# Kernel tuning notes

Hardware: AMD Instinct MI355X
Metric: run time of the kernel (lower is better)

## Reference

```python
import jax, jax.numpy as jnp
import numpy as np

B, S, D, H, AD, E = 4, 2048, 1024, 2048, 128, 8

def _ln(x, g, b, eps=1e-5):
    m = jnp.mean(x, axis=-1, keepdims=True)
    v = jnp.var(x, axis=-1, keepdims=True)
    return (x - m) * jax.lax.rsqrt(v + eps) * g + b

def setup_inputs() -> dict:
    key = jax.random.key(0)
    ks = jax.random.split(key, 12)
    scale = 1.0 / D ** 0.5
    ascale = scale * 0.01
    ead = 0.01 / AD ** 0.5
    return {
        'x': jax.random.normal(ks[0], (B, S, D), jnp.float32),
        'expert_weights': jax.random.uniform(ks[1], (B, S, E), jnp.float32),
        'Wu': jax.random.normal(ks[2], (H, D), jnp.float32) * scale,
        'bu': jnp.zeros((H,), jnp.float32),
        'Wg': jax.random.normal(ks[3], (H, D), jnp.float32) * scale,
        'bg': jnp.zeros((H,), jnp.float32),
        'Wd': jax.random.normal(ks[4], (D, H), jnp.float32) * scale,
        'bd': jnp.zeros((D,), jnp.float32),
        'Wpre': jax.random.normal(ks[5], (AD, D), jnp.float32) * ascale,
        'bpre': jnp.zeros((AD,), jnp.float32),
        'Wpost': jax.random.normal(ks[6], (AD, H), jnp.float32) * ascale,
        'bpost': jnp.zeros((AD,), jnp.float32),
        'ln_g': jnp.ones((AD,), jnp.float32),
        'ln_b': jnp.zeros((AD,), jnp.float32),
        'Wap': jax.random.normal(ks[7], (H, AD), jnp.float32) * ascale,
        'A': jax.random.normal(ks[8], (E, AD, AD), jnp.float32) * ead,
        'eg': jnp.ones((E, AD), jnp.float32),
        'eb': jnp.zeros((E, AD), jnp.float32),
        'Wp': jax.random.normal(ks[9], (H, AD), jnp.float32) * ead,
        'Wo': jax.random.normal(ks[10], (D, H), jnp.float32) * ead,
    }

def reference(x, expert_weights, Wu, bu, Wg, bg, Wd, bd, Wpre, bpre, Wpost, bpost, ln_g, ln_b, Wap, A, eg, eb, Wp, Wo):
    # ---- SharedExpertMLP ----
    up = x @ Wu.T + bu                      # [B,S,H]
    gate = x @ Wg.T + bg
    hidden = jax.nn.silu(gate) * up
    adapt_in = _ln(x @ Wpre.T + bpre, ln_g, ln_b)        # [B,S,AD]
    adapt_out = _ln(hidden @ Wpost.T + bpost, ln_g, ln_b)
    aw = jnp.einsum('bsa,bta->bst', adapt_in, adapt_out)  # [B,S,S]
    aw = jax.nn.silu(jnp.clip(aw, -5.0, 5.0))
    adapt = jnp.einsum('bst,bta->bsa', aw, adapt_in)
    hidden = hidden + 0.1 * (adapt @ Wap.T)
    shared = hidden @ Wd.T + bd                           # [B,S,D]
    # ---- expert branch (vectorized over experts) ----
    pre = x @ Wpre.T + bpre                               # [B,S,AD] (no adapt_norm here, as in torch)
    h = jnp.einsum('bsa,eca->ebsc', pre, A)               # per-expert adapter linear
    h = _ln(h, eg[:, None, None, :], eb[:, None, None, :])
    wmask = jnp.where(expert_weights > 0, expert_weights, 0.0)  # [B,S,E]
    hw = jnp.einsum('ebsa,bse->bsa', h, wmask)            # weighted combine before shared projections
    Wc = Wo @ Wp                                          # [D,AD]: output_proj(expert_proj(.))
    contrib = hw @ Wc.T                                   # [B,S,D]
    # sum_i w_i * (shared + 0.1*mask_i*expert_i) = shared*sum(w) + 0.1*sum(w_i*expert_i)
    return shared * jnp.sum(expert_weights, axis=-1, keepdims=True) + 0.1 * contrib
```

## Files before the change

kernel.cpp:

```cpp
#include <hip/hip_runtime.h>
#include <math.h>

#define BB 4
#define SS 2048
#define DD 1024
#define HH 2048
#define AD 128
#define EE 8
#define MM (BB*SS)
#define PS 136

typedef unsigned short u16;
typedef short bf16x8 __attribute__((ext_vector_type(8)));
typedef float f32x4 __attribute__((ext_vector_type(4)));
typedef float f32x16 __attribute__((ext_vector_type(16)));

__device__ __forceinline__ float silu_f(float x){ return x / (1.f + __expf(-x)); }

__device__ __forceinline__ u16 f2bf(float f){
    union { float f; unsigned u; } c; c.f = f;
    unsigned r = (c.u + 0x7FFFu + ((c.u >> 16) & 1u)) >> 16;
    return (u16)r;
}

__device__ __forceinline__ void gld16(const u16* g, u16* l){
    __builtin_amdgcn_global_load_lds((const __attribute__((address_space(1))) void*)g,
                                     (__attribute__((address_space(3))) void*)l, 16, 0, 0);
}

__global__ __launch_bounds__(256,2) void mfma_sk(
    const u16* __restrict__ A, const u16* __restrict__ B, float* __restrict__ P,
    int M, int K, int S, long sA, long sB, long sC, long sSplit)
{
    __shared__ __align__(16) u16 As[128*32];
    __shared__ __align__(16) u16 Bs[128*32];
    const int t = threadIdx.x;
    const int lane = t & 63;
    const int wv = t >> 6;
    const int s = blockIdx.x;
    const int m0 = blockIdx.y * 128;
    const u16* Ab = A + (long)blockIdx.z * sA;
    const u16* Bb = B + (long)blockIdx.z * sB;
    const int srow = t >> 2, scol = (t & 3) * 8;
    const int Ks = K / S, kBeg = s * Ks;
    const u16* ga0 = Ab + (long)(m0 + srow) * K + scol + kBeg;
    const u16* ga1 = ga0 + 64L * K;
    const u16* gb0 = Bb + (long)srow * K + scol + kBeg;
    const u16* gb1 = gb0 + 64L * K;
    u16* la0 = As + t * 8;  u16* la1 = As + 2048 + t * 8;
    u16* lb0 = Bs + t * 8;  u16* lb1 = Bs + 2048 + t * 8;
    const int fr = lane & 15, q = lane >> 4;
    const int wm = (wv & 1) * 64, wn = (wv >> 1) * 64;

    f32x4 acc[4][4] = {};
    for (int k0 = 0; k0 < Ks; k0 += 32) {
        gld16(ga0 + k0, la0);
        gld16(ga1 + k0, la1);
        gld16(gb0 + k0, lb0);
        gld16(gb1 + k0, lb1);
        __syncthreads();
        bf16x8 af[4], bfr[4];
        #pragma unroll
        for (int i = 0; i < 4; ++i) af[i]  = *(const bf16x8*)&As[(wm + i*16 + fr)*32 + q*8];
        #pragma unroll
        for (int i = 0; i < 4; ++i) bfr[i] = *(const bf16x8*)&Bs[(wn + i*16 + fr)*32 + q*8];
        #pragma unroll
        for (int mi = 0; mi < 4; ++mi)
            #pragma unroll
            for (int ni = 0; ni < 4; ++ni)
                acc[mi][ni] = __builtin_amdgcn_mfma_f32_16x16x32_bf16(af[mi], bfr[ni], acc[mi][ni], 0, 0, 0);
        __syncthreads();
    }

    float* Pf = P + (long)s * sSplit + (long)blockIdx.z * sC;
    #pragma unroll
    for (int mi = 0; mi < 4; ++mi)
        #pragma unroll
        for (int ni = 0; ni < 4; ++ni) {
            const int col = wn + ni*16 + fr;
            #pragma unroll
            for (int r = 0; r < 4; ++r) {
                const int row = m0 + wm + mi*16 + q*4 + r;
                Pf[(long)row * 128 + col] = acc[mi][ni][r];
            }
        }
}

__global__ __launch_bounds__(256,2) void mfma_upgate(
    const u16* __restrict__ X, const u16* __restrict__ Wu_, const u16* __restrict__ Wg_,
    const float* __restrict__ bu, const float* __restrict__ bg, u16* __restrict__ H)
{
    __shared__ __align__(16) u16 Xs[128*32];
    __shared__ __align__(16) u16 Us[128*32];
    __shared__ __align__(16) u16 Gs[128*32];
    const int t = threadIdx.x, lane = t & 63, wv = t >> 6;
    const int m0 = blockIdx.y * 128, n0 = blockIdx.x * 128;
    const int srow = t >> 2, scol = (t & 3) * 8;
    const u16* gx0 = X   + (long)(m0 + srow) * DD + scol;
    const u16* gx1 = gx0 + 64L * DD;
    const u16* gu0 = Wu_ + (long)(n0 + srow) * DD + scol;
    const u16* gu1 = gu0 + 64L * DD;
    const u16* gg0 = Wg_ + (long)(n0 + srow) * DD + scol;
    const u16* gg1 = gg0 + 64L * DD;
    const int l31 = lane & 31, kh = lane >> 5;
    const int wm = (wv & 1) * 64, wn = (wv >> 1) * 64;

    f32x16 accu[2][2] = {};
    f32x16 accg[2][2] = {};
    for (int k0 = 0; k0 < DD; k0 += 32) {
        gld16(gx0 + k0, Xs + t*8);
        gld16(gx1 + k0, Xs + 2048 + t*8);
        gld16(gu0 + k0, Us + t*8);
        gld16(gu1 + k0, Us + 2048 + t*8);
        gld16(gg0 + k0, Gs + t*8);
        gld16(gg1 + k0, Gs + 2048 + t*8);
        __syncthreads();
        bf16x8 xf[2][2], uf[2][2], gf[2][2];
        #pragma unroll
        for (int mt = 0; mt < 2; ++mt)
            #pragma unroll
            for (int ks = 0; ks < 2; ++ks) {
                xf[mt][ks] = *(const bf16x8*)&Xs[(wm + mt*32 + l31)*32 + ks*16 + kh*8];
                uf[mt][ks] = *(const bf16x8*)&Us[(wn + mt*32 + l31)*32 + ks*16 + kh*8];
                gf[mt][ks] = *(const bf16x8*)&Gs[(wn + mt*32 + l31)*32 + ks*16 + kh*8];
            }
        #pragma unroll
        for (int mt = 0; mt < 2; ++mt)
            #pragma unroll
            for (int nt = 0; nt < 2; ++nt)
                #pragma unroll
                for (int ks = 0; ks < 2; ++ks) {
                    accu[mt][nt] = __builtin_amdgcn_mfma_f32_32x32x16_bf16(xf[mt][ks], uf[nt][ks], accu[mt][nt], 0, 0, 0);
                    accg[mt][nt] = __builtin_amdgcn_mfma_f32_32x32x16_bf16(xf[mt][ks], gf[nt][ks], accg[mt][nt], 0, 0, 0);
                }
        __syncthreads();
    }
    #pragma unroll
    for (int mt = 0; mt < 2; ++mt)
        #pragma unroll
        for (int nt = 0; nt < 2; ++nt) {
            const int col = n0 + wn + nt*32 + l31;
            #pragma unroll
            for (int r = 0; r < 16; ++r) {
                const int row = m0 + wm + mt*32 + (r & 3) + 8*(r >> 2) + 4*kh;
                const float u = accu[mt][nt][r] + bu[col];
                const float g = accg[mt][nt][r] + bg[col];
                H[(long)row * HH + col] = f2bf(silu_f(g) * u);
            }
        }
}

__global__ __launch_bounds__(256,2) void mfma_final(
    const u16* __restrict__ Hh, const u16* __restrict__ Wd_,
    const u16* __restrict__ Ac, const u16* __restrict__ Wcat,
    const float* __restrict__ bd, const float* __restrict__ sumw,
    float* __restrict__ out)
{
    __shared__ __align__(16) u16 As[128*32];
    __shared__ __align__(16) u16 Bs[128*32];
    const int t = threadIdx.x, lane = t & 63, wv = t >> 6;
    const int m0 = blockIdx.y * 128, n0 = blockIdx.x * 128;
    const int srow = t >> 2, scol = (t & 3) * 8;
    const int l31 = lane & 31, kh = lane >> 5;
    const int wm = (wv & 1) * 64, wn = (wv >> 1) * 64;
    u16* la0 = As + t * 8;  u16* la1 = As + 2048 + t * 8;
    u16* lb0 = Bs + t * 8;  u16* lb1 = Bs + 2048 + t * 8;

    f32x16 acc[2][2] = {};
    {
        const u16* ga0 = Hh  + (long)(m0 + srow) * HH + scol;
        const u16* ga1 = ga0 + 64L * HH;
        const u16* gb0 = Wd_ + (long)(n0 + srow) * HH + scol;
        const u16* gb1 = gb0 + 64L * HH;
        for (int k0 = 0; k0 < HH; k0 += 32) {
            gld16(ga0 + k0, la0);
            gld16(ga1 + k0, la1);
            gld16(gb0 + k0, lb0);
            gld16(gb1 + k0, lb1);
            __syncthreads();
            bf16x8 af[2][2], bf[2][2];
            #pragma unroll
            for (int mt = 0; mt < 2; ++mt)
                #pragma unroll
                for (int ks = 0; ks < 2; ++ks) {
                    af[mt][ks] = *(const bf16x8*)&As[(wm + mt*32 + l31)*32 + ks*16 + kh*8];
                    bf[mt][ks] = *(const bf16x8*)&Bs[(wn + mt*32 + l31)*32 + ks*16 + kh*8];
                }
            #pragma unroll
            for (int mt = 0; mt < 2; ++mt)
                #pragma unroll
                for (int nt = 0; nt < 2; ++nt)
                    #pragma unroll
                    for (int ks = 0; ks < 2; ++ks)
                        acc[mt][nt] = __builtin_amdgcn_mfma_f32_32x32x16_bf16(af[mt][ks], bf[nt][ks], acc[mt][nt], 0, 0, 0);
            __syncthreads();
        }
    }
    f32x16 acc2[2][2] = {};
    {
        const u16* ga0 = Ac   + (long)(m0 + srow) * 256 + scol;
        const u16* ga1 = ga0 + 64L * 256;
        const u16* gb0 = Wcat + (long)(n0 + srow) * 256 + scol;
        const u16* gb1 = gb0 + 64L * 256;
        for (int k0 = 0; k0 < 256; k0 += 32) {
            gld16(ga0 + k0, la0);
            gld16(ga1 + k0, la1);
            gld16(gb0 + k0, lb0);
            gld16(gb1 + k0, lb1);
            __syncthreads();
            bf16x8 af[2][2], bf[2][2];
            #pragma unroll
            for (int mt = 0; mt < 2; ++mt)
                #pragma unroll
                for (int ks = 0; ks < 2; ++ks) {
                    af[mt][ks] = *(const bf16x8*)&As[(wm + mt*32 + l31)*32 + ks*16 + kh*8];
                    bf[mt][ks] = *(const bf16x8*)&Bs[(wn + mt*32 + l31)*32 + ks*16 + kh*8];
                }
            #pragma unroll
            for (int mt = 0; mt < 2; ++mt)
                #pragma unroll
                for (int nt = 0; nt < 2; ++nt)
                    #pragma unroll
                    for (int ks = 0; ks < 2; ++ks)
                        acc2[mt][nt] = __builtin_amdgcn_mfma_f32_32x32x16_bf16(af[mt][ks], bf[nt][ks], acc2[mt][nt], 0, 0, 0);
            __syncthreads();
        }
    }
    #pragma unroll
    for (int mt = 0; mt < 2; ++mt)
        #pragma unroll
        for (int nt = 0; nt < 2; ++nt) {
            const int col = n0 + wn + nt*32 + l31;
            #pragma unroll
            for (int r = 0; r < 16; ++r) {
                const int row = m0 + wm + mt*32 + (r & 3) + 8*(r >> 2) + 4*kh;
                out[(long)row * DD + col] =
                    sumw[row] * (acc[mt][nt][r] + bd[col]) + 0.1f * acc2[mt][nt][r];
            }
        }
}

__global__ __launch_bounds__(256,2) void flash_pv(
    const u16* __restrict__ ai, const u16* __restrict__ ao,
    const u16* __restrict__ aiT, float* __restrict__ adaptP)
{
    __shared__ __align__(16) u16 As[128*32];
    __shared__ __align__(16) u16 Bs[128*32];
    __shared__ __align__(16) u16 Psh[128*PS];
    const int t = threadIdx.x, lane = t & 63, wv = t >> 6;
    const int fr = lane & 15, q = lane >> 4;
    const int wm = (wv & 1) * 64, wn = (wv >> 1) * 64;
    const int tg = blockIdx.x, s0 = blockIdx.y * 128, b = blockIdx.z;
    const u16* aib  = ai  + (long)b * SS * AD;
    const u16* aob  = ao  + (long)b * SS * AD;
    const u16* aiTb = aiT + (long)b * AD * SS;
    const int srow = t >> 2, scol = (t & 3) * 8;
    u16* la0 = As + t * 8;  u16* la1 = As + 2048 + t * 8;
    u16* lb0 = Bs + t * 8;  u16* lb1 = Bs + 2048 + t * 8;
    const u16* ga0 = aib + (long)(s0 + srow) * AD + scol;
    const u16* ga1 = ga0 + 64L * AD;

    f32x4 vacc[4][4] = {};
    for (int ti = 0; ti < 2; ++ti) {
        const int t0 = tg * 256 + ti * 128;
        const u16* gb0 = aob + (long)(t0 + srow) * AD + scol;
        const u16* gb1 = gb0 + 64L * AD;
        f32x4 acc[4][4] = {};
        for (int k0 = 0; k0 < AD; k0 += 32) {
            gld16(ga0 + k0, la0);
            gld16(ga1 + k0, la1);
            gld16(gb0 + k0, lb0);
            gld16(gb1 + k0, lb1);
            __syncthreads();
            bf16x8 af[4], bfr[4];
            #pragma unroll
            for (int i = 0; i < 4; ++i) af[i]  = *(const bf16x8*)&As[(wm + i*16 + fr)*32 + q*8];
            #pragma unroll
            for (int i = 0; i < 4; ++i) bfr[i] = *(const bf16x8*)&Bs[(wn + i*16 + fr)*32 + q*8];
            #pragma unroll
            for (int mi = 0; mi < 4; ++mi)
                #pragma unroll
                for (int ni = 0; ni < 4; ++ni)
                    acc[mi][ni] = __builtin_amdgcn_mfma_f32_16x16x32_bf16(af[mi], bfr[ni], acc[mi][ni], 0, 0, 0);
            __syncthreads();
        }
        #pragma unroll
        for (int mi = 0; mi < 4; ++mi)
            #pragma unroll
            for (int ni = 0; ni < 4; ++ni)
                #pragma unroll
                for (int r = 0; r < 4; ++r) {
                    float v = acc[mi][ni][r];
                    v = fminf(fmaxf(v, -5.f), 5.f);
                    Psh[(wm + mi*16 + q*4 + r)*PS + wn + ni*16 + fr] = f2bf(silu_f(v));
                }
        __syncthreads();
        #pragma unroll
        for (int kk = 0; kk < 4; ++kk) {
            bf16x8 pf[4], bi[4];
            #pragma unroll
            for (int mi = 0; mi < 4; ++mi)
                pf[mi] = *(const bf16x8*)&Psh[(wm + mi*16 + fr)*PS + kk*32 + q*8];
            #pragma unroll
            for (int ni = 0; ni < 4; ++ni)
                bi[ni] = *(const bf16x8*)&aiTb[(long)(wn + ni*16 + fr)*SS + t0 + kk*32 + q*8];
            #pragma unroll
            for (int mi = 0; mi < 4; ++mi)
                #pragma unroll
                for (int ni = 0; ni < 4; ++ni)
                    vacc[mi][ni] = __builtin_amdgcn_mfma_f32_16x16x32_bf16(pf[mi], bi[ni], vacc[mi][ni], 0, 0, 0);
        }
    }
    float* Pf = adaptP + (long)tg * MM * AD + (long)(b * SS + s0) * AD;
    #pragma unroll
    for (int mi = 0; mi < 4; ++mi)
        #pragma unroll
        for (int ni = 0; ni < 4; ++ni) {
            const int col = wn + ni*16 + fr;
            #pragma unroll
            for (int r = 0; r < 4; ++r) {
                const int row = wm + mi*16 + q*4 + r;
                Pf[(long)row * AD + col] = vacc[mi][ni][r];
            }
        }
}

__global__ __launch_bounds__(256) void scale_adapt(
    const float* __restrict__ P, const float* __restrict__ sumw, u16* __restrict__ acat)
{
    const int i = blockIdx.x * 256 + threadIdx.x;
    float4 v = ((const float4*)P)[i];
    #pragma unroll
    for (int tg = 1; tg < 8; ++tg) {
        const float4 w = ((const float4*)P)[i + (long)tg * (MM*AD/4)];
        v.x += w.x; v.y += w.y; v.z += w.z; v.w += w.w;
    }
    const long grow = i >> 5;
    const float sw = sumw[grow];
    ushort4 o;
    o.x = f2bf(sw*v.x); o.y = f2bf(sw*v.y); o.z = f2bf(sw*v.z); o.w = f2bf(sw*v.w);
    ((ushort4*)acat)[grow*64 + 32 + (i & 31)] = o;
}

__global__ __launch_bounds__(256) void expert_fused(
    const u16* __restrict__ pre, const u16* __restrict__ aexp,
    const float* __restrict__ ew, const float* __restrict__ eg,
    const float* __restrict__ eb, u16* __restrict__ acat,
    float* __restrict__ sumw)
{
    __shared__ float ewsh[64*8];
    __shared__ float egsh[8*128], ebsh[8*128];
    const int t = threadIdx.x, lane = t & 63, wv = t >> 6;
    const int fr = lane & 15, q = lane >> 4;
    const int wm = wv * 16;
    const int m0 = blockIdx.x * 64;
    if (t < 128) {
        const int row = t >> 1, j = (t & 1)*4;
        *(float4*)&ewsh[row*8+j] = *(const float4*)&ew[(long)(m0+row)*EE + j];
    }
    {   const int e = t >> 5, c = (t & 31)*4;
        *(float4*)&egsh[e*128+c] = *(const float4*)&eg[e*128+c];
        *(float4*)&ebsh[e*128+c] = *(const float4*)&eb[e*128+c]; }
    __syncthreads();

    f32x4 hwacc[8] = {};
    for (int e = 0; e < EE; ++e) {
        f32x4 acc[8] = {};
        const u16* Ae = aexp + (long)e * AD * AD;
        #pragma unroll
        for (int ks = 0; ks < 4; ++ks) {
            bf16x8 af, bfr[8];
            af = *(const bf16x8*)&pre[(long)(m0 + wm + fr)*AD + ks*32 + q*8];
            #pragma unroll
            for (int ni = 0; ni < 8; ++ni)
                bfr[ni] = *(const bf16x8*)&Ae[(long)(ni*16 + fr)*AD + ks*32 + q*8];
            #pragma unroll
            for (int ni = 0; ni < 8; ++ni)
                acc[ni] = __builtin_amdgcn_mfma_f32_16x16x32_bf16(af, bfr[ni], acc[ni], 0, 0, 0);
        }
        #pragma unroll
        for (int r = 0; r < 4; ++r) {
            float s = 0.f, s2 = 0.f;
            #pragma unroll
            for (int ni = 0; ni < 8; ++ni) { const float v = acc[ni][r]; s += v; s2 += v*v; }
            #pragma unroll
            for (int msk = 1; msk < 16; msk <<= 1) {
                s  += __shfl_xor(s,  msk, 64);
                s2 += __shfl_xor(s2, msk, 64);
            }
            const float mean = s * (1.f/128.f);
            const float var  = s2 * (1.f/128.f) - mean*mean;
            const float rs   = rsqrtf(var + 1e-5f);
            const int rowl = wm + q*4 + r;
            float w = ewsh[rowl*8 + e]; w = w > 0.f ? w : 0.f;
            #pragma unroll
            for (int ni = 0; ni < 8; ++ni) {
                const int col = ni*16 + fr;
                hwacc[ni][r] += w * ((acc[ni][r] - mean) * rs * egsh[e*128+col] + ebsh[e*128+col]);
            }
        }
    }
    #pragma unroll
    for (int r = 0; r < 4; ++r) {
        const int rowl = wm + q*4 + r;
        #pragma unroll
        for (int ni = 0; ni < 8; ++ni)
            acat[(long)(m0+rowl)*256 + ni*16 + fr] = f2bf(hwacc[ni][r]);
        if (fr == 0) {
            float sw = 0.f;
            #pragma unroll
            for (int j = 0; j < 8; ++j) sw += ewsh[rowl*8 + j];
            sumw[m0 + rowl] = sw;
        }
    }
}

template<int S>
__global__ __launch_bounds__(128) void ln_reduce(
    const float* __restrict__ P, long sSplit, const float* __restrict__ bias,
    u16* __restrict__ raw, u16* __restrict__ ln_out,
    const float* __restrict__ g, const float* __restrict__ b)
{
    const int r = blockIdx.x, tid = threadIdx.x;
    float v = bias[tid];
    #pragma unroll
    for (int s = 0; s < S; ++s) v += P[(long)s * sSplit + (long)r * AD + tid];
    if (raw) raw[(long)r * AD + tid] = f2bf(v);
    __shared__ float red[AD], red2[AD];
    red[tid] = v; red2[tid] = v*v;
    __syncthreads();
    for (int s = 64; s > 0; s >>= 1) {
        if (tid < s) { red[tid] += red[tid+s]; red2[tid] += red2[tid+s]; }
        __syncthreads();
    }
    const float mean = red[0] * (1.f/AD);
    const float var  = red2[0] * (1.f/AD) - mean*mean;
    const float rs   = rsqrtf(var + 1e-5f);
    ln_out[(long)r * AD + tid] = f2bf((v - mean) * rs * g[tid] + b[tid]);
}

__global__ __launch_bounds__(256) void reduce_cat(
    const float* __restrict__ P, u16* __restrict__ Wcat)
{
    const int i = blockIdx.x * 256 + threadIdx.x;
    const int a4 = i & 31, z = (i >> 5) & 1, d = i >> 6;
    const float* src = P + (long)z * (4L*DD*AD) + (long)d * AD + a4*4;
    float4 v = *(const float4*)src;
    #pragma unroll
    for (int s = 1; s < 4; ++s) {
        const float4 w = *(const float4*)(src + (long)s * DD * AD);
        v.x += w.x; v.y += w.y; v.z += w.z; v.w += w.w;
    }
    ushort4 o; o.x=f2bf(v.x); o.y=f2bf(v.y); o.z=f2bf(v.z); o.w=f2bf(v.w);
    ((ushort4*)Wcat)[(long)d*64 + z*32 + a4] = o;
}

__global__ __launch_bounds__(256) void transpose6(
    const u16* __restrict__ wRaw, u16* __restrict__ wT,
    const u16* __restrict__ ai, u16* __restrict__ aiT)
{
    __shared__ u16 tile[32][33];
    const int z = blockIdx.z;
    const u16* in; u16* out;
    if (z < 2) { in = wRaw + (long)z * HH * AD; out = wT + (long)z * AD * HH; }
    else       { in = ai + (long)(z-2) * SS * AD; out = aiT + (long)(z-2) * AD * SS; }
    const int x0 = blockIdx.x * 32, y0 = blockIdx.y * 32;
    const int tx = threadIdx.x & 31, ty = threadIdx.x >> 5;
    #pragma unroll
    for (int j = 0; j < 4; ++j)
        tile[ty + j*8][tx] = in[(long)(y0 + ty + j*8) * AD + x0 + tx];
    __syncthreads();
    #pragma unroll
    for (int j = 0; j < 4; ++j)
        out[(long)(x0 + ty + j*8) * SS + y0 + tx] = tile[tx][ty + j*8];
}

struct Cvt5 { const float* in[5]; u16* out[5]; long cum[6]; };
__global__ __launch_bounds__(256) void cvt_pack(Cvt5 a)
{
    const long i = (long)blockIdx.x * 256 + threadIdx.x;
    if (i >= a.cum[5]) return;
    int s = 0;
    while (i >= a.cum[s+1]) ++s;
    const long j = i - a.cum[s];
    const float4 v = ((const float4*)a.in[s])[j];
    ushort4 o;
    o.x = f2bf(v.x); o.y = f2bf(v.y); o.z = f2bf(v.z); o.w = f2bf(v.w);
    ((ushort4*)a.out[s])[j] = o;
}

extern "C" void kernel_launch(void* const* d_in, const int* in_sizes, int n_in,
                              void* d_out, int out_size, void* d_ws, size_t ws_size,
                              hipStream_t stream) {
    const float* x    = (const float*)d_in[0];
    const float* ew   = (const float*)d_in[1];
    const float* Wu   = (const float*)d_in[2];
    const float* bu   = (const float*)d_in[3];
    const float* Wg   = (const float*)d_in[4];
    const float* bg   = (const float*)d_in[5];
    const float* Wd   = (const float*)d_in[6];
    const float* bd   = (const float*)d_in[7];
    const float* Wpre = (const float*)d_in[8];
    const float* bpre = (const float*)d_in[9];
    const float* Wpost= (const float*)d_in[10];
    const float* bpost= (const float*)d_in[11];
    const float* ln_g = (const float*)d_in[12];
    const float* ln_b = (const float*)d_in[13];
    const float* Wap  = (const float*)d_in[14];
    const float* Aex  = (const float*)d_in[15];
    const float* eg   = (const float*)d_in[16];
    const float* eb   = (const float*)d_in[17];
    const float* Wp   = (const float*)d_in[18];
    const float* Wo   = (const float*)d_in[19];
    float* out = (float*)d_out;

    char* p = (char*)d_ws;
    auto take = [&](long bytes) -> char* {
        char* r = p; p += (bytes + 255) & ~255L; return r;
    };
    u16* x_slot  = (u16*)take(16777216);
    u16* wslot   = (u16*)take((long)2*DD*HH*2);
    u16* wpre    = (u16*)take((long)AD*DD*2);
    u16* aex     = (u16*)take((long)EE*AD*AD*2);
    u16* pre_bf  = (u16*)take((long)MM*AD*2);
    u16* ai_bf   = (u16*)take((long)MM*AD*2);
    char* shareA = take(33554432);
    u16* acat    = (u16*)take((long)MM*256*2);
    float* sumw  = (float*)take((long)MM*4);
    u16* hidden  = (u16*)take((long)MM*HH*2);

    u16* x_bf    = x_slot;
    u16* aiT     = x_slot;
    u16* wRaw    = aiT  + 1048576;
    u16* wT      = wRaw + 524288;
    u16* wpost_w = wT   + 524288;
    u16* wcat    = wpost_w + 262144;
    u16* ao_bf   = wcat + 262144;
    float* wcP   = (float*)(ao_bf + 1048576);
    float* preP   = (float*)shareA;
    float* wpostP = (float*)shareA;
    float* adaptP = (float*)shareA;

    {
        Cvt5 a;
        a.in[0]=x;    a.out[0]=x_bf;              long n0=(long)MM*DD/4;
        a.in[1]=Wu;   a.out[1]=wslot;             long n1=(long)HH*DD/4;
        a.in[2]=Wg;   a.out[2]=wslot+(long)DD*HH; long n2=(long)HH*DD/4;
        a.in[3]=Wpre; a.out[3]=wpre;              long n3=(long)AD*DD/4;
        a.in[4]=Aex;  a.out[4]=aex;               long n4=(long)EE*AD*AD/4;
        a.cum[0]=0; a.cum[1]=n0; a.cum[2]=n0+n1; a.cum[3]=n0+n1+n2;
        a.cum[4]=n0+n1+n2+n3; a.cum[5]=n0+n1+n2+n3+n4;
        cvt_pack<<<dim3((a.cum[5]+255)/256), 256, 0, stream>>>(a);
    }
    mfma_sk<<<dim3(4, MM/128, 1), 256, 0, stream>>>(
        x_bf, wpre, preP, MM, DD, 4, 0, 0, 0, (long)MM*AD);
    ln_reduce<4><<<dim3(MM), 128, 0, stream>>>(preP, (long)MM*AD, bpre, pre_bf, ai_bf, ln_g, ln_b);
    expert_fused<<<dim3(MM/64), 256, 0, stream>>>(pre_bf, aex, ew, eg, eb, acat, sumw);
    mfma_upgate<<<dim3(HH/128, MM/128, 1), 256, 0, stream>>>(
        x_bf, wslot, wslot+(long)DD*HH, bu, bg, hidden);
    {
        Cvt5 a;
        a.in[0]=Wo;    a.out[0]=wslot;             long n0=(long)DD*HH/4;
        a.in[1]=Wd;    a.out[1]=wslot+(long)DD*HH; long n1=(long)DD*HH/4;
        a.in[2]=Wpost; a.out[2]=wpost_w;           long n2=(long)AD*HH/4;
        a.in[3]=Wp;    a.out[3]=wRaw;              long n3=(long)HH*AD/4;
        a.in[4]=Wap;   a.out[4]=wRaw+(long)HH*AD;  long n4=(long)HH*AD/4;
        a.cum[0]=0; a.cum[1]=n0; a.cum[2]=n0+n1; a.cum[3]=n0+n1+n2;
        a.cum[4]=n0+n1+n2+n3; a.cum[5]=n0+n1+n2+n3+n4;
        cvt_pack<<<dim3((a.cum[5]+255)/256), 256, 0, stream>>>(a);
    }
    transpose6<<<dim3(4,64,6), 256, 0, stream>>>(wRaw, wT, ai_bf, aiT);
    mfma_sk<<<dim3(4, DD/128, 2), 256, 0, stream>>>(
        wslot, wT, wcP, DD, HH, 4, (long)DD*HH, (long)AD*HH, 4L*DD*AD, (long)DD*AD);
    reduce_cat<<<dim3(256), 256, 0, stream>>>(wcP, wcat);
    mfma_sk<<<dim3(8, MM/128, 1), 256, 0, stream>>>(
        hidden, wpost_w, wpostP, MM, HH, 8, 0, 0, 0, (long)MM*AD);
    ln_reduce<8><<<dim3(MM), 128, 0, stream>>>(wpostP, (long)MM*AD, bpost, nullptr, ao_bf, ln_g, ln_b);
    flash_pv<<<dim3(8, SS/128, BB), 256, 0, stream>>>(ai_bf, ao_bf, aiT, adaptP);
    scale_adapt<<<dim3((long)MM*AD/4/256), 256, 0, stream>>>(adaptP, sumw, acat);
    mfma_final<<<dim3(DD/128, MM/128), 256, 0, stream>>>(
        hidden, wslot+(long)DD*HH, acat, wcat, bd, sumw, out);
}
```

Before: 437.7 us.

## Pipeline up/gate GEMM with 4-stage LDS ring, swizzle, larger tiles

Rewrites the fused up/gate GEMM kernel to use 512-thread blocks over 256x128 output tiles. Global-to-LDS loads go through a four-buffer ring with three tiles in flight, and explicit vmcnt waits plus a single barrier per k-step replace the two syncthreads per iteration. LDS columns are XOR-swizzled to avoid bank conflicts, and MFMA issue priority is raised. The aim is to hide memory latency and raise MFMA utilisation, at the cost of 128 KB of LDS per block, which limits occupancy, and a fragile hand-counted vmcnt schedule.

```diff
diff --git a/kernel.cpp b/kernel.cpp
--- a/kernel.cpp
+++ b/kernel.cpp
@@ -27,6 +27,8 @@
     __builtin_amdgcn_global_load_lds((const __attribute__((address_space(1))) void*)g,
                                      (__attribute__((address_space(3))) void*)l, 16, 0, 0);
 }
+
+#define VMCNT(n) asm volatile("s_waitcnt vmcnt(" #n ")" ::: "memory")
 
 __global__ __launch_bounds__(256,2) void mfma_sk(
     const u16* __restrict__ A, const u16* __restrict__ B, float* __restrict__ P,
@@ -86,67 +88,105 @@
         }
 }
 
-__global__ __launch_bounds__(256,2) void mfma_upgate(
+__global__ __launch_bounds__(512,2) void mfma_upgate(
     const u16* __restrict__ X, const u16* __restrict__ Wu_, const u16* __restrict__ Wg_,
     const float* __restrict__ bu, const float* __restrict__ bg, u16* __restrict__ H)
 {
-    __shared__ __align__(16) u16 Xs[128*32];
-    __shared__ __align__(16) u16 Us[128*32];
-    __shared__ __align__(16) u16 Gs[128*32];
+    __shared__ __align__(16) u16 lds[65536];
     const int t = threadIdx.x, lane = t & 63, wv = t >> 6;
-    const int m0 = blockIdx.y * 128, n0 = blockIdx.x * 128;
-    const int srow = t >> 2, scol = (t & 3) * 8;
-    const u16* gx0 = X   + (long)(m0 + srow) * DD + scol;
-    const u16* gx1 = gx0 + 64L * DD;
-    const u16* gu0 = Wu_ + (long)(n0 + srow) * DD + scol;
-    const u16* gu1 = gu0 + 64L * DD;
-    const u16* gg0 = Wg_ + (long)(n0 + srow) * DD + scol;
-    const u16* gg1 = gg0 + 64L * DD;
     const int l31 = lane & 31, kh = lane >> 5;
-    const int wm = (wv & 1) * 64, wn = (wv >> 1) * 64;
-
-    f32x16 accu[2][2] = {};
-    f32x16 accg[2][2] = {};
-    for (int k0 = 0; k0 < DD; k0 += 32) {
-        gld16(gx0 + k0, Xs + t*8);
-        gld16(gx1 + k0, Xs + 2048 + t*8);
-        gld16(gu0 + k0, Us + t*8);
-        gld16(gu1 + k0, Us + 2048 + t*8);
-        gld16(gg0 + k0, Gs + t*8);
-        gld16(gg1 + k0, Gs + 2048 + t*8);
-        __syncthreads();
-        bf16x8 xf[2][2], uf[2][2], gf[2][2];
-        #pragma unroll
-        for (int mt = 0; mt < 2; ++mt)
+    const int wr = wv >> 2, wc = wv & 3;
+    const int m0 = blockIdx.y * 256, n0 = blockIdx.x * 128;
+
+    const int srow = t >> 2;
+    const int gcol = (((t & 3) ^ ((t >> 3) & 3)) * 8);
+    const u16* gx0 = X   + (long)(m0 + srow) * DD + gcol;
+    const u16* gx1 = gx0 + 128L * DD;
+    const u16* gu  = Wu_ + (long)(n0 + srow) * DD + gcol;
+    const u16* gg  = Wg_ + (long)(n0 + srow) * DD + gcol;
+    const int st8 = t * 8;
+
+    const int sw3 = (l31 >> 1) & 3;
+    int offA[4][2], offB[2];
+    #pragma unroll
+    for (int m = 0; m < 4; ++m)
+        #pragma unroll
+        for (int ks = 0; ks < 2; ++ks)
+            offA[m][ks] = (wr*128 + m*32 + l31)*32 + (((ks*2 + kh) ^ sw3) * 8);
+    #pragma unroll
+    for (int ks = 0; ks < 2; ++ks)
+        offB[ks] = (wc*32 + l31)*32 + (((ks*2 + kh) ^ sw3) * 8);
+
+    f32x16 accU[4] = {};
+    f32x16 accG[4] = {};
+
+    auto stage = [&](int tb) {
+        u16* Lb = lds + (tb & 3) * 16384;
+        const int k0 = tb * 32;
+        gld16(gx0 + k0, Lb + st8);
+        gld16(gx1 + k0, Lb + 4096 + st8);
+        gld16(gu  + k0, Lb + 8192 + st8);
+        gld16(gg  + k0, Lb + 12288 + st8);
+    };
+
+    auto compute = [&](int tb) {
+        const u16* Lb = lds + (tb & 3) * 16384;
+        bf16x8 a[4][2], uf[2], gf[2];
+        #pragma unroll
+        for (int ks = 0; ks < 2; ++ks) {
+            uf[ks] = *(const bf16x8*)&Lb[8192  + offB[ks]];
+            gf[ks] = *(const bf16x8*)&Lb[12288 + offB[ks]];
+        }
+        #pragma unroll
+        for (int m = 0; m < 4; ++m)
+            #pragma unroll
+            for (int ks = 0; ks < 2; ++ks)
+                a[m][ks] = *(const bf16x8*)&Lb[offA[m][ks]];
+        __builtin_amdgcn_s_setprio(1);
+        #pragma unroll
+        for (int m = 0; m < 4; ++m)
             #pragma unroll
             for (int ks = 0; ks < 2; ++ks) {
-                xf[mt][ks] = *(const bf16x8*)&Xs[(wm + mt*32 + l31)*32 + ks*16 + kh*8];
-                uf[mt][ks] = *(const bf16x8*)&Us[(wn + mt*32 + l31)*32 + ks*16 + kh*8];
-                gf[mt][ks] = *(const bf16x8*)&Gs[(wn + mt*32 + l31)*32 + ks*16 + kh*8];
+                accU[m] = __builtin_amdgcn_mfma_f32_32x32x16_bf16(a[m][ks], uf[ks], accU[m], 0, 0, 0);
+                accG[m] = __builtin_amdgcn_mfma_f32_32x32x16_bf16(a[m][ks], gf[ks], accG[m], 0, 0, 0);
             }
-        #pragma unroll
-        for (int mt = 0; mt < 2; ++mt)
-            #pragma unroll
-            for (int nt = 0; nt < 2; ++nt)
-                #pragma unroll
-                for (int ks = 0; ks < 2; ++ks) {
-                    accu[mt][nt] = __builtin_amdgcn_mfma_f32_32x32x16_bf16(xf[mt][ks], uf[nt][ks], accu[mt][nt], 0, 0, 0);
-                    accg[mt][nt] = __builtin_amdgcn_mfma_f32_32x32x16_bf16(xf[mt][ks], gf[nt][ks], accg[mt][nt], 0, 0, 0);
-                }
-        __syncthreads();
-    }
-    #pragma unroll
-    for (int mt = 0; mt < 2; ++mt)
-        #pragma unroll
-        for (int nt = 0; nt < 2; ++nt) {
-            const int col = n0 + wn + nt*32 + l31;
-            #pragma unroll
-            for (int r = 0; r < 16; ++r) {
-                const int row = m0 + wm + mt*32 + (r & 3) + 8*(r >> 2) + 4*kh;
-                const float u = accu[mt][nt][r] + bu[col];
-                const float g = accg[mt][nt][r] + bg[col];
-                H[(long)row * HH + col] = f2bf(silu_f(g) * u);
-            }
+        __builtin_amdgcn_s_setprio(0);
+    };
+
+    stage(0); stage(1); stage(2);
+
+    #pragma unroll 1
+    for (int tt = 0; tt < 29; ++tt) {
+        VMCNT(8);
+        __builtin_amdgcn_s_barrier();
+        __builtin_amdgcn_sched_barrier(0);
+        stage(tt + 3);
+        compute(tt);
+    }
+    VMCNT(8);
+    __builtin_amdgcn_s_barrier();
+    __builtin_amdgcn_sched_barrier(0);
+    compute(29);
+    VMCNT(4);
+    __builtin_amdgcn_s_barrier();
+    __builtin_amdgcn_sched_barrier(0);
+    compute(30);
+    VMCNT(0);
+    __builtin_amdgcn_s_barrier();
+    __builtin_amdgcn_sched_barrier(0);
+    compute(31);
+
+    const int col = n0 + wc*32 + l31;
+    const float bub = bu[col], bgb = bg[col];
+    u16* Hp = H + (long)(m0 + wr*128) * HH + col;
+    #pragma unroll
+    for (int m = 0; m < 4; ++m)
+        #pragma unroll
+        for (int r = 0; r < 16; ++r) {
+            const int rowl = m*32 + (r & 3) + 8*(r >> 2) + 4*kh;
+            const float u = accU[m][r] + bub;
+            const float g = accG[m][r] + bgb;
+            Hp[(long)rowl * HH] = f2bf(silu_f(g) * u);
         }
 }
 
@@ -556,7 +596,7 @@
         x_bf, wpre, preP, MM, DD, 4, 0, 0, 0, (long)MM*AD);
     ln_reduce<4><<<dim3(MM), 128, 0, stream>>>(preP, (long)MM*AD, bpre, pre_bf, ai_bf, ln_g, ln_b);
     expert_fused<<<dim3(MM/64), 256, 0, stream>>>(pre_bf, aex, ew, eg, eb, acat, sumw);
-    mfma_upgate<<<dim3(HH/128, MM/128, 1), 256, 0, stream>>>(
+    mfma_upgate<<<dim3(HH/128, MM/256), 512, 0, stream>>>(
         x_bf, wslot, wslot+(long)DD*HH, bu, bg, hidden);
     {
         Cvt5 a;
```

Result: no change. 430.8 us (-1.6%).
